# Performance work log

Measured on AMD Instinct MI355X. Metric: run time of the kernel, lower is better.

The kernel has to match this reference:

```python
import jax, jax.numpy as jnp
import numpy as np

D_MODEL = 512
NUM_HEADS = 8
HEAD_DIM = D_MODEL // NUM_HEADS  # 64
EMBEDDING_DIM = 512  # undefined global EmbeddingDim in source -> d_model
EVENT_DIM = 388      # undefined global EventDim in source -> MIDI event vocab
B, T = 2, 2048


def setup_inputs() -> dict:
    key = jax.random.key(0)
    ks = jax.random.split(key, 12)
    sc = 0.02
    v = jax.random.normal(ks[0], (B, T, D_MODEL), jnp.float32)
    k = jax.random.normal(ks[1], (B, T, D_MODEL), jnp.float32)
    q = jax.random.normal(ks[2], (B, T, D_MODEL), jnp.float32)
    mask = jnp.tril(jnp.ones((T, T), jnp.float32))  # causal mask, broadcasts to [H,B,T,T]
    Wq = jax.random.normal(ks[3], (D_MODEL, HEAD_DIM), jnp.float32) * sc
    bq = jnp.zeros((HEAD_DIM,), jnp.float32)
    Wk = jax.random.normal(ks[4], (D_MODEL, HEAD_DIM), jnp.float32) * sc
    bk = jnp.zeros((HEAD_DIM,), jnp.float32)
    Wv = jax.random.normal(ks[5], (D_MODEL, HEAD_DIM), jnp.float32) * sc
    bv = jnp.zeros((HEAD_DIM,), jnp.float32)
    E = jax.random.normal(ks[6], (NUM_HEADS, T, HEAD_DIM), jnp.float32) * sc
    Wo = jax.random.normal(ks[7], (D_MODEL, EMBEDDING_DIM), jnp.float32) * sc
    bo = jnp.zeros((EMBEDDING_DIM,), jnp.float32)
    Wl = jax.random.normal(ks[8], (EMBEDDING_DIM, EVENT_DIM), jnp.float32) * sc
    bl = jnp.zeros((EVENT_DIM,), jnp.float32)
    return {"v": v, "k": k, "q": q, "mask": mask, "Wq": Wq, "bq": bq,
            "Wk": Wk, "bk": bk, "Wv": Wv, "bv": bv, "E": E,
            "Wo": Wo, "bo": bo, "Wl": Wl, "bl": bl}


def _skew(S):
    # S: [H,B,T,T] -> Music-Transformer skew via left-pad, reshape, slice
    H, Bb, Tt, _ = S.shape
    S = jnp.pad(S, ((0, 0), (0, 0), (0, 0), (1, 0)))          # [H,B,T,T+1]
    S = S.reshape(H, Bb, Tt + 1, Tt)                           # [H,B,T+1,T]
    return S[:, :, 1:]                                         # [H,B,T,T]


def reference(v, k, q, mask, Wq, bq, Wk, bk, Wv, bv, E, Wo, bo, Wl, bl):
    # The source applies the SAME Dense per head, so all heads share q/k/v projections
    qh = q @ Wq + bq  # [B,T,hd]
    kh = k @ Wk + bk  # [B,T,hd]
    vh = v @ Wv + bv  # [B,T,hd]
    # relative-position scores per head: Q @ E^T then skew
    S = jnp.einsum('btd,hsd->hbts', qh, E)  # [H,B,T,T]
    S = _skew(S)
    qk = jnp.einsum('btd,bsd->bts', qh, kh)  # [B,T,T], identical across heads
    attn = (qk[None] + S) / np.sqrt(HEAD_DIM)  # [H,B,T,T]
    attn = attn * mask - jnp.asarray(1e10, attn.dtype) * (1.0 - mask)
    score = jax.nn.softmax(attn, axis=-1)
    ctx = jnp.einsum('hbts,bsd->hbtd', score, vh)  # [H,B,T,hd]
    ctx = jnp.transpose(ctx, (1, 2, 0, 3)).reshape(ctx.shape[1], ctx.shape[2], -1)  # [B,T,d_model]
    ctx = jax.nn.relu(ctx @ Wo + bo)  # [B,T,EmbeddingDim]
    logits = ctx @ Wl + bl            # [B,T,EventDim]
    return logits
```

## Files before the change

kernel.cpp:

```cpp
#include <hip/hip_runtime.h>
#include <hip/hip_bf16.h>


#define B_ 2
#define T_ 2048
#define DM_ 512
#define H_ 8
#define HD_ 64
#define ED_ 512
#define EV_ 388
#define BT_ (B_ * T_)

typedef __attribute__((ext_vector_type(8))) short short8;
typedef __attribute__((ext_vector_type(4))) float floatx4;

#define MFMA(a, b, c) __builtin_amdgcn_mfma_f32_16x16x32_bf16((a), (b), (c), 0, 0, 0)

__device__ __forceinline__ float bfs(unsigned short s) {
  union { unsigned int i; float f; } v; v.i = ((unsigned int)s) << 16; return v.f;
}
__device__ __forceinline__ unsigned short f2bf(float f) {
  __hip_bfloat16 h = __float2bfloat16(f);
  union { __hip_bfloat16 h; unsigned short u; } v; v.h = h; return v.u;
}
__device__ __forceinline__ float ldf(const void* p, int i, bool isbf) {
  return isbf ? bfs(((const unsigned short*)p)[i]) : ((const float*)p)[i];
}
__device__ __forceinline__ bool det_bf(const unsigned int* mask) {
  return mask[0] != 0x3F800000u;
}
__device__ __forceinline__ void gl_lds16(const unsigned short* g, void* l) {
  __builtin_amdgcn_global_load_lds(
      (const __attribute__((address_space(1))) void*)g,
      (__attribute__((address_space(3))) void*)l, 16, 0, 0);
}

__global__ __launch_bounds__(256) void prep_kernel(
    const void* __restrict__ E, const void* __restrict__ Wq,
    const void* __restrict__ Wk, const void* __restrict__ Wv,
    const void* __restrict__ Wo, const void* __restrict__ Wl,
    const unsigned int* __restrict__ mask,
    unsigned short* __restrict__ E_c, unsigned short* __restrict__ WqT,
    unsigned short* __restrict__ WkT, unsigned short* __restrict__ WvT,
    unsigned short* __restrict__ WoT, unsigned short* __restrict__ WlT) {
  const bool isbf = det_bf(mask);
  const int tid = threadIdx.x;
  int bi = blockIdx.x;
  if (bi < 1024) {
    const int i0 = (bi * 256 + tid) * 4;
    if (isbf) {
      *(uint2*)&E_c[i0] = *(const uint2*)((const unsigned short*)E + i0);
    } else {
      float4 f = *(const float4*)((const float*)E + i0);
      unsigned short p[4] = {f2bf(f.x), f2bf(f.y), f2bf(f.z), f2bf(f.w)};
      *(uint2*)&E_c[i0] = *(uint2*)p;
    }
    return;
  }
  bi -= 1024;
  const void* src; unsigned short* dst; int N, nb;
  if (bi < 16)       { src = Wq; dst = WqT; N = 64;  nb = bi; }
  else if (bi < 32)  { src = Wk; dst = WkT; N = 64;  nb = bi - 16; }
  else if (bi < 48)  { src = Wv; dst = WvT; N = 64;  nb = bi - 32; }
  else if (bi < 176) { src = Wo; dst = WoT; N = 512; nb = bi - 48; }
  else               { src = Wl; dst = WlT; N = 388; nb = bi - 176; }
  const int n = nb * 4 + (tid >> 6);
  const int k0 = (tid & 63) * 8;
  unsigned short vv[8];
#pragma unroll
  for (int j = 0; j < 8; ++j) {
    if (n >= N) vv[j] = 0;
    else if (isbf) vv[j] = ((const unsigned short*)src)[(size_t)(k0 + j) * N + n];
    else vv[j] = f2bf(((const float*)src)[(size_t)(k0 + j) * N + n]);
  }
  *(uint4*)&dst[(size_t)n * DM_ + k0] = *(uint4*)vv;
}

__global__ __launch_bounds__(256) void gemm_proj(
    const void* __restrict__ xq, const void* __restrict__ xk,
    const void* __restrict__ xv,
    const unsigned short* __restrict__ WqT, const unsigned short* __restrict__ WkT,
    const unsigned short* __restrict__ WvT,
    const void* __restrict__ bq, const void* __restrict__ bk,
    const void* __restrict__ bv, const unsigned int* __restrict__ mask,
    unsigned short* __restrict__ oq, unsigned short* __restrict__ ok,
    unsigned short* __restrict__ ovt) {
  __shared__ __align__(16) short sA[64][72];
  __shared__ __align__(16) short sW[64][72];
  const int sel = blockIdx.y;
  const void* x = (sel == 0) ? xq : (sel == 1) ? xk : xv;
  const unsigned short* WT = (sel == 0) ? WqT : (sel == 1) ? WkT : WvT;
  const void* bias = (sel == 0) ? bq : (sel == 1) ? bk : bv;
  const bool isbf = det_bf(mask);

  const int tid = threadIdx.x;
  const int w = tid >> 6, lane = tid & 63;
  const int q_ = lane >> 4, n_ = lane & 15;
  const int row0 = blockIdx.x * 64;

  floatx4 acc[4];
#pragma unroll
  for (int j = 0; j < 4; ++j) acc[j] = (floatx4){0.f, 0.f, 0.f, 0.f};

  for (int k0 = 0; k0 < DM_; k0 += 64) {
    if (isbf) {
#pragma unroll
      for (int it = 0; it < 2; ++it) {
        int idx = tid + it * 256;
        int rr = idx >> 3, cc = (idx & 7) * 8;
        *(uint4*)&sA[rr][cc] =
            *(const uint4*)((const unsigned short*)x + (size_t)(row0 + rr) * DM_ + k0 + cc);
      }
    } else {
#pragma unroll
      for (int it = 0; it < 4; ++it) {
        int idx = tid + it * 256;
        int rr = idx >> 4, cc = (idx & 15) * 4;
        float4 f = *(const float4*)((const float*)x + (size_t)(row0 + rr) * DM_ + k0 + cc);
        unsigned short p[4] = {f2bf(f.x), f2bf(f.y), f2bf(f.z), f2bf(f.w)};
        *(uint2*)&sA[rr][cc] = *(uint2*)p;
      }
    }
#pragma unroll
    for (int it = 0; it < 2; ++it) {
      int idx = tid + it * 256;
      int rr = idx >> 3, cc = (idx & 7) * 8;
      *(uint4*)&sW[rr][cc] = *(const uint4*)(WT + (size_t)rr * DM_ + k0 + cc);
    }
    __syncthreads();
    short8 a0 = *(const short8*)&sA[16 * w + n_][8 * q_];
    short8 a1 = *(const short8*)&sA[16 * w + n_][32 + 8 * q_];
#pragma unroll
    for (int nb = 0; nb < 4; ++nb) {
      short8 b0 = *(const short8*)&sW[16 * nb + n_][8 * q_];
      short8 b1 = *(const short8*)&sW[16 * nb + n_][32 + 8 * q_];
      acc[nb] = MFMA(a0, b0, acc[nb]);
      acc[nb] = MFMA(a1, b1, acc[nb]);
    }
    __syncthreads();
  }

#pragma unroll
  for (int nb = 0; nb < 4; ++nb) {
    const int col = 16 * nb + n_;
    const float bb = ldf(bias, col, isbf);
#pragma unroll
    for (int r = 0; r < 4; ++r) {
      int row = row0 + 16 * w + 4 * q_ + r;
      unsigned short val = f2bf(acc[nb][r] + bb);
      if (sel < 2) {
        unsigned short* o = (sel == 0) ? oq : ok;
        o[(size_t)row * HD_ + col] = val;
      } else {
        int b = row >> 11, s = row & 2047;
        ovt[(((size_t)(b * HD_ + col)) << 11) + s] = val;
      }
    }
  }
}

__device__ __forceinline__ int pbase_of(int ti) {
  return (ti < 16) ? (ti - 8) * 2 : (ti < 24) ? 16 + (ti - 16) * 3
                                              : 40 + (ti - 24) * 4;
}

__global__ __launch_bounds__(256, 2) void attn_kernel(
    const unsigned short* __restrict__ qh, const unsigned short* __restrict__ kh,
    const unsigned short* __restrict__ vt, const unsigned short* __restrict__ E,
    unsigned short* __restrict__ ctxo, float* __restrict__ pc,
    float* __restrict__ ml) {
  __shared__ __align__(16) short sK[2][64][64];
  __shared__ __align__(16) short sVT[2][64][64];
  __shared__ __align__(16) short sE[2][128][64];
  __shared__ __align__(16) short sP[64][64];

  const int id = blockIdx.x;
  const int hb = id & 15;
  const int rem = 79 - (id >> 4);
  int ti, c, nc;
  if (rem < 8)       { ti = rem;                 c = 0;            nc = 1; }
  else if (rem < 24) { ti = 8 + ((rem - 8) >> 1);  c = (rem - 8) & 1;  nc = 2; }
  else if (rem < 48) { ti = 16 + (rem - 24) / 3;   c = (rem - 24) % 3; nc = 3; }
  else               { ti = 24 + ((rem - 48) >> 2); c = (rem - 48) & 3; nc = 4; }
  const int nsteps = ti + 1;
  const int klo = (c * nsteps) / nc;
  const int khi = ((c + 1) * nsteps) / nc;

  const int h = hb >> 1, b = hb & 1;
  const int t0 = ti * 64;

  const int tid = threadIdx.x;
  const int w = tid >> 6, lane = tid & 63;
  const int q_ = lane >> 4, n_ = lane & 15;

  const int trow = t0 + 16 * w + n_;
  const unsigned short* qp = qh + (((size_t)((b << 11) + trow)) << 6) + (q_ << 3);
  const short8 qa0 = *(const short8*)qp;
  const short8 qa1 = *(const short8*)(qp + 32);

  short8 onesf;
#pragma unroll
  for (int j = 0; j < 8; ++j) onesf[j] = (short)0x3F80;

  floatx4 ctxa[4];
#pragma unroll
  for (int nb = 0; nb < 4; ++nb) ctxa[nb] = (floatx4){0.f, 0.f, 0.f, 0.f};
  floatx4 lacc = (floatx4){0.f, 0.f, 0.f, 0.f};

  const unsigned short* eb = E + ((size_t)h << 17);
  const unsigned short* kbase = kh + (((size_t)(b << 11)) << 6);
  const unsigned short* vbase = vt + (((size_t)(b << 6)) << 11);

  const int lrow8 = lane >> 3;
  const int lch = ((lane & 7) ^ lrow8) << 3;
  const int rK0 = 8 * w + lrow8;
  const int c0s = ((q_ ^ (n_ & 7)) << 3);
  const int c1s = (((q_ | 4) ^ (n_ & 7)) << 3);

#define STAGE(bufsel, s0v)                                                     \
  {                                                                            \
    const unsigned short* gK =                                                 \
        kbase + (((size_t)((s0v) + rK0)) << 6) + lch;                          \
    const unsigned short* gV =                                                 \
        vbase + (((size_t)rK0) << 11) + (s0v) + lch;                           \
    gl_lds16(gK, (void*)&sK[bufsel][8 * w][0]);                                \
    gl_lds16(gK + (32 << 6), (void*)(&sK[bufsel][8 * w][0] + 32 * 64));        \
    gl_lds16(gV, (void*)&sVT[bufsel][8 * w][0]);                               \
    gl_lds16(gV + (32 << 11), (void*)(&sVT[bufsel][8 * w][0] + 32 * 64));      \
    const int rbE = (T_ - 64) + (s0v)-t0;                                      \
    _Pragma("unroll") for (int off = 0; off < 4; ++off) {                      \
      int gr = rbE + 32 * w + 8 * off + lrow8;                                 \
      if (gr > T_ - 1) gr = T_ - 1;           \
      gl_lds16(eb + ((size_t)gr << 6) + lch,                                   \
               (void*)&sE[bufsel][32 * w + 8 * off][0]);                       \
    }                                                                          \
  }

  STAGE(0, klo * 64);

  for (int kt = klo; kt < khi; ++kt) {
    const int cur = (kt - klo) & 1;
    const int s0 = kt * 64;

    asm volatile("s_waitcnt vmcnt(0)" ::: "memory");
    __builtin_amdgcn_sched_barrier(0);
    __builtin_amdgcn_s_barrier();
    __builtin_amdgcn_sched_barrier(0);

    if (kt + 1 < khi) STAGE(cur ^ 1, s0 + 64);

    floatx4 qk[4];
    __builtin_amdgcn_s_setprio(1);
#pragma unroll
    for (int nb = 0; nb < 4; ++nb) {
      short8 kb0 = *(const short8*)&sK[cur][16 * nb + n_][c0s];
      short8 kb1 = *(const short8*)&sK[cur][16 * nb + n_][c1s];
      qk[nb] = (floatx4){0.f, 0.f, 0.f, 0.f};
      qk[nb] = MFMA(qa0, kb0, qk[nb]);
      qk[nb] = MFMA(qa1, kb1, qk[nb]);
    }
    floatx4 qe[5];
#pragma unroll
    for (int f = 0; f < 5; ++f) {
      const short* ep = &sE[cur][16 * (3 - w + f) + n_][0];
      short8 eb0 = *(const short8*)(ep + c0s);
      short8 eb1 = *(const short8*)(ep + c1s);
      qe[f] = (floatx4){0.f, 0.f, 0.f, 0.f};
      qe[f] = MFMA(qa0, eb0, qe[f]);
      qe[f] = MFMA(qa1, eb1, qe[f]);
    }
    __builtin_amdgcn_s_setprio(0);

    const bool diag = (kt == ti);
#pragma unroll
    for (int r = 0; r < 4; ++r) {
      const int t = 4 * q_ + r;
      const int ba = ((q_ << 4) | ((n_ - t + 15) & 15)) << 2;
      const int nd = (n_ + t + 1) & 15;
      const bool hi = nd > t;
      const int swr = (t & 7) << 3;
#pragma unroll
      for (int mb = 0; mb < 4; ++mb) {
        float merged = hi ? qe[mb + 1][r] : qe[mb][r];
        float g = __int_as_float(
            __builtin_amdgcn_ds_bpermute(ba, __float_as_int(merged)));
        float sv = qk[mb][r] + g;
        if (diag && (16 * mb + n_ > 16 * w + t)) sv = -1.0e30f;
        sP[16 * w + t][(16 * mb + n_) ^ swr] =
            (short)f2bf(exp2f(sv * 0.18033688011f));
      }
    }

    short8 pa0 = *(const short8*)&sP[16 * w + n_][c0s];
    short8 pa1 = *(const short8*)&sP[16 * w + n_][c1s];
    __builtin_amdgcn_s_setprio(1);
#pragma unroll
    for (int nb = 0; nb < 4; ++nb) {
      short8 v0 = *(const short8*)&sVT[cur][16 * nb + n_][c0s];
      short8 v1 = *(const short8*)&sVT[cur][16 * nb + n_][c1s];
      ctxa[nb] = MFMA(pa0, v0, ctxa[nb]);
      ctxa[nb] = MFMA(pa1, v1, ctxa[nb]);
    }
    lacc = MFMA(pa0, onesf, lacc);
    lacc = MFMA(pa1, onesf, lacc);
    __builtin_amdgcn_s_setprio(0);
  }
#undef STAGE

  if (nc == 1) {
#pragma unroll
    for (int r = 0; r < 4; ++r) {
      const float inv = 1.0f / lacc[r];
      const int row = t0 + 16 * w + 4 * q_ + r;
      const size_t base = (((size_t)((b << 11) + row)) << 9) + (h << 6) + n_;
#pragma unroll
      for (int nb = 0; nb < 4; ++nb)
        ctxo[base + 16 * nb] = f2bf(ctxa[nb][r] * inv);
    }
  } else {
    const int idx = hb * 72 + pbase_of(ti) + c;
    float* pcb = pc + ((size_t)idx << 12);
    float* mlb = ml + ((size_t)idx << 6);
#pragma unroll
    for (int r = 0; r < 4; ++r) {
      const int row = 16 * w + 4 * q_ + r;
#pragma unroll
      for (int nb = 0; nb < 4; ++nb)
        pcb[(row << 6) + 16 * nb + n_] = ctxa[nb][r];
      if (n_ == 0) mlb[row] = lacc[r];
    }
  }
}

__global__ __launch_bounds__(256) void combine_kernel(
    const float* __restrict__ pc, const float* __restrict__ ml,
    unsigned short* __restrict__ ctxo) {
  const int cb = blockIdx.x;
  const int hb = cb / 24;
  const int ti = 8 + cb % 24;
  const int nc = (ti >> 3) + 1;
  const int h = hb >> 1, b = hb & 1, t0 = ti * 64;
  const int tid = threadIdx.x;
  const int row = tid >> 2, seg = (tid & 3) * 16;
  const int idx0 = hb * 72 + pbase_of(ti);

  float lsum = 0.f;
  float4 a4[4];
#pragma unroll
  for (int j = 0; j < 4; ++j) a4[j] = (float4){0.f, 0.f, 0.f, 0.f};
  for (int c = 0; c < nc; ++c) {
    const int idx = idx0 + c;
    lsum += ml[((size_t)idx << 6) + row];
    const float* cp = pc + ((size_t)idx << 12) + (row << 6) + seg;
#pragma unroll
    for (int j = 0; j < 4; ++j) {
      float4 x = *(const float4*)(cp + 4 * j);
      a4[j].x += x.x; a4[j].y += x.y; a4[j].z += x.z; a4[j].w += x.w;
    }
  }
  const float inv = 1.0f / lsum;
  unsigned short o[16];
#pragma unroll
  for (int j = 0; j < 4; ++j) {
    o[4 * j + 0] = f2bf(a4[j].x * inv);
    o[4 * j + 1] = f2bf(a4[j].y * inv);
    o[4 * j + 2] = f2bf(a4[j].z * inv);
    o[4 * j + 3] = f2bf(a4[j].w * inv);
  }
  unsigned short* dst =
      ctxo + (((size_t)((b << 11) + t0 + row)) << 9) + (h << 6) + seg;
  *(uint4*)dst = *(uint4*)&o[0];
  *(uint4*)(dst + 8) = *(uint4*)&o[8];
}

template <int RELU>
__global__ __launch_bounds__(256) void mlp_mfma(
    const unsigned short* __restrict__ A, const unsigned short* __restrict__ WT,
    const void* __restrict__ bias, unsigned short* __restrict__ outBF,
    void* __restrict__ outD, const unsigned int* __restrict__ mask) {
  __shared__ __align__(16) short sA[64][72];
  __shared__ __align__(16) short sW[64][72];
  const int tid = threadIdx.x;
  const int w = tid >> 6, lane = tid & 63;
  const int q_ = lane >> 4, n_ = lane & 15;
  const int row0 = blockIdx.x * 64;
  const int n0 = blockIdx.y * 64;
  const bool isbf = det_bf(mask);

  floatx4 acc[4];
#pragma unroll
  for (int j = 0; j < 4; ++j) acc[j] = (floatx4){0.f, 0.f, 0.f, 0.f};

  for (int k0 = 0; k0 < DM_; k0 += 64) {
#pragma unroll
    for (int it = 0; it < 2; ++it) {
      int idx = tid + it * 256;
      int rr = idx >> 3, cc = (idx & 7) * 8;
      *(uint4*)&sA[rr][cc] = *(const uint4*)(A + (size_t)(row0 + rr) * DM_ + k0 + cc);
      *(uint4*)&sW[rr][cc] = *(const uint4*)(WT + (size_t)(n0 + rr) * DM_ + k0 + cc);
    }
    __syncthreads();
    short8 a0 = *(const short8*)&sA[16 * w + n_][8 * q_];
    short8 a1 = *(const short8*)&sA[16 * w + n_][32 + 8 * q_];
#pragma unroll
    for (int nb = 0; nb < 4; ++nb) {
      short8 b0 = *(const short8*)&sW[16 * nb + n_][8 * q_];
      short8 b1 = *(const short8*)&sW[16 * nb + n_][32 + 8 * q_];
      acc[nb] = MFMA(a0, b0, acc[nb]);
      acc[nb] = MFMA(a1, b1, acc[nb]);
    }
    __syncthreads();
  }

#pragma unroll
  for (int nb = 0; nb < 4; ++nb) {
    const int col = n0 + 16 * nb + n_;
    float bb = 0.f;
    if (RELU || col < EV_) bb = ldf(bias, col, isbf);
#pragma unroll
    for (int r = 0; r < 4; ++r) {
      const int row = row0 + 16 * w + 4 * q_ + r;
      float v = acc[nb][r] + bb;
      if (RELU) {
        outBF[(size_t)row * ED_ + col] = f2bf(fmaxf(v, 0.f));
      } else if (col < EV_) {
        if (isbf) ((unsigned short*)outD)[(size_t)row * EV_ + col] = f2bf(v);
        else      ((float*)outD)[(size_t)row * EV_ + col] = v;
      }
    }
  }
}

extern "C" void kernel_launch(void* const* d_in, const int* in_sizes, int n_in,
                              void* d_out, int out_size, void* d_ws, size_t ws_size,
                              hipStream_t stream) {
  const void* v  = d_in[0];
  const void* k  = d_in[1];
  const void* q  = d_in[2];
  const unsigned int* mask = (const unsigned int*)d_in[3];
  const void* Wq = d_in[4];
  const void* bq = d_in[5];
  const void* Wk = d_in[6];
  const void* bk = d_in[7];
  const void* Wv = d_in[8];
  const void* bv = d_in[9];
  const void* E  = d_in[10];
  const void* Wo = d_in[11];
  const void* bo = d_in[12];
  const void* Wl = d_in[13];
  const void* bl = d_in[14];

  char* p = (char*)d_ws;
  unsigned short* E_c  = (unsigned short*)p; p += (size_t)H_ * T_ * HD_ * 2;
  unsigned short* qhb  = (unsigned short*)p; p += (size_t)BT_ * HD_ * 2;
  unsigned short* khb  = (unsigned short*)p; p += (size_t)BT_ * HD_ * 2;
  unsigned short* vtb  = (unsigned short*)p; p += (size_t)BT_ * HD_ * 2;
  unsigned short* WqT  = (unsigned short*)p; p += (size_t)HD_ * DM_ * 2;
  unsigned short* WkT  = (unsigned short*)p; p += (size_t)HD_ * DM_ * 2;
  unsigned short* WvT  = (unsigned short*)p; p += (size_t)HD_ * DM_ * 2;
  unsigned short* WoT  = (unsigned short*)p; p += (size_t)ED_ * DM_ * 2;
  unsigned short* WlT  = (unsigned short*)p; p += (size_t)448 * DM_ * 2;
  unsigned short* ctxb = (unsigned short*)p; p += (size_t)BT_ * DM_ * 2;
  unsigned short* h1b  = (unsigned short*)p; p += (size_t)BT_ * ED_ * 2;
  float* pc = (float*)p; p += (size_t)16 * 72 * 4096 * 4;
  float* ml = (float*)p; p += (size_t)16 * 72 * 64 * 4;

  prep_kernel<<<dim3(1312), 256, 0, stream>>>(
      E, Wq, Wk, Wv, Wo, Wl, mask, E_c, WqT, WkT, WvT, WoT, WlT);
  gemm_proj<<<dim3(BT_ / 64, 3), 256, 0, stream>>>(
      q, k, v, WqT, WkT, WvT, bq, bk, bv, mask, qhb, khb, vtb);
  attn_kernel<<<dim3(1280), 256, 0, stream>>>(qhb, khb, vtb, E_c, ctxb, pc, ml);
  combine_kernel<<<dim3(384), 256, 0, stream>>>(pc, ml, ctxb);
  mlp_mfma<1><<<dim3(BT_ / 64, ED_ / 64), 256, 0, stream>>>(
      ctxb, WoT, bo, h1b, nullptr, mask);
  mlp_mfma<0><<<dim3(BT_ / 64, 448 / 64), 256, 0, stream>>>(
      h1b, WlT, bl, nullptr, d_out, mask);
}
```

Measured before the change: 202.5 us.

## Load K/V fragments directly from global and rebalance attention split-K partitioning

K and V^T fragments are now read straight from global memory into registers instead of being staged through double-buffered LDS, which shrinks LDS use and lets the launch bound rise to 4 blocks per SM. The split-K partitioning of query tiles is reworked to at most 3 chunks, and block order is no longer reversed to launch the longest tiles first, so fewer blocks and a smaller partial buffer feed the combine kernel. The risk is higher global and L2 traffic and latency exposed on every MFMA operand load, since nothing prefetches these loads now, and worse tail balance.

After: 235.9 us. 1.17x slower.

```diff
diff --git a/kernel.cpp b/kernel.cpp
--- a/kernel.cpp
+++ b/kernel.cpp
@@ -160,28 +160,24 @@
 }
 
 __device__ __forceinline__ int pbase_of(int ti) {
-  return (ti < 16) ? (ti - 8) * 2 : (ti < 24) ? 16 + (ti - 16) * 3
-                                              : 40 + (ti - 24) * 4;
-}
-
-__global__ __launch_bounds__(256, 2) void attn_kernel(
+  return (ti < 22) ? (ti - 11) * 2 : 22 + (ti - 22) * 3;
+}
+
+__global__ __launch_bounds__(256, 4) void attn_kernel(
     const unsigned short* __restrict__ qh, const unsigned short* __restrict__ kh,
     const unsigned short* __restrict__ vt, const unsigned short* __restrict__ E,
     unsigned short* __restrict__ ctxo, float* __restrict__ pc,
     float* __restrict__ ml) {
-  __shared__ __align__(16) short sK[2][64][64];
-  __shared__ __align__(16) short sVT[2][64][64];
   __shared__ __align__(16) short sE[2][128][64];
   __shared__ __align__(16) short sP[64][64];
 
   const int id = blockIdx.x;
   const int hb = id & 15;
-  const int rem = 79 - (id >> 4);
+  const int rem = id >> 4;
   int ti, c, nc;
-  if (rem < 8)       { ti = rem;                 c = 0;            nc = 1; }
-  else if (rem < 24) { ti = 8 + ((rem - 8) >> 1);  c = (rem - 8) & 1;  nc = 2; }
-  else if (rem < 48) { ti = 16 + (rem - 24) / 3;   c = (rem - 24) % 3; nc = 3; }
-  else               { ti = 24 + ((rem - 48) >> 2); c = (rem - 48) & 3; nc = 4; }
+  if (rem < 11)      { ti = rem;                  c = 0;              nc = 1; }
+  else if (rem < 33) { ti = 11 + ((rem - 11) >> 1); c = (rem - 11) & 1; nc = 2; }
+  else               { ti = 22 + (rem - 33) / 3;    c = (rem - 33) % 3; nc = 3; }
   const int nsteps = ti + 1;
   const int klo = (c * nsteps) / nc;
   const int khi = ((c + 1) * nsteps) / nc;
@@ -208,25 +204,16 @@
   floatx4 lacc = (floatx4){0.f, 0.f, 0.f, 0.f};
 
   const unsigned short* eb = E + ((size_t)h << 17);
-  const unsigned short* kbase = kh + (((size_t)(b << 11)) << 6);
-  const unsigned short* vbase = vt + (((size_t)(b << 6)) << 11);
+  const unsigned short* kfr = kh + (((size_t)(b << 11) + n_) << 6) + (q_ << 3);
+  const unsigned short* vfr = vt + (((size_t)((b << 6) + n_)) << 11) + (q_ << 3);
 
   const int lrow8 = lane >> 3;
   const int lch = ((lane & 7) ^ lrow8) << 3;
-  const int rK0 = 8 * w + lrow8;
   const int c0s = ((q_ ^ (n_ & 7)) << 3);
   const int c1s = (((q_ | 4) ^ (n_ & 7)) << 3);
 
 #define STAGE(bufsel, s0v)                                                     \
   {                                                                            \
-    const unsigned short* gK =                                                 \
-        kbase + (((size_t)((s0v) + rK0)) << 6) + lch;                          \
-    const unsigned short* gV =                                                 \
-        vbase + (((size_t)rK0) << 11) + (s0v) + lch;                           \
-    gl_lds16(gK, (void*)&sK[bufsel][8 * w][0]);                                \
-    gl_lds16(gK + (32 << 6), (void*)(&sK[bufsel][8 * w][0] + 32 * 64));        \
-    gl_lds16(gV, (void*)&sVT[bufsel][8 * w][0]);                               \
-    gl_lds16(gV + (32 << 11), (void*)(&sVT[bufsel][8 * w][0] + 32 * 64));      \
     const int rbE = (T_ - 64) + (s0v)-t0;                                      \
     _Pragma("unroll") for (int off = 0; off < 4; ++off) {                      \
       int gr = rbE + 32 * w + 8 * off + lrow8;                                 \
@@ -253,8 +240,9 @@
     __builtin_amdgcn_s_setprio(1);
 #pragma unroll
     for (int nb = 0; nb < 4; ++nb) {
-      short8 kb0 = *(const short8*)&sK[cur][16 * nb + n_][c0s];
-      short8 kb1 = *(const short8*)&sK[cur][16 * nb + n_][c1s];
+      const unsigned short* kp = kfr + (((size_t)(s0 + 16 * nb)) << 6);
+      short8 kb0 = *(const short8*)kp;
+      short8 kb1 = *(const short8*)(kp + 32);
       qk[nb] = (floatx4){0.f, 0.f, 0.f, 0.f};
       qk[nb] = MFMA(qa0, kb0, qk[nb]);
       qk[nb] = MFMA(qa1, kb1, qk[nb]);
@@ -296,8 +284,9 @@
     __builtin_amdgcn_s_setprio(1);
 #pragma unroll
     for (int nb = 0; nb < 4; ++nb) {
-      short8 v0 = *(const short8*)&sVT[cur][16 * nb + n_][c0s];
-      short8 v1 = *(const short8*)&sVT[cur][16 * nb + n_][c1s];
+      const unsigned short* vp = vfr + (((size_t)(16 * nb)) << 11) + s0;
+      short8 v0 = *(const short8*)vp;
+      short8 v1 = *(const short8*)(vp + 32);
       ctxa[nb] = MFMA(pa0, v0, ctxa[nb]);
       ctxa[nb] = MFMA(pa1, v1, ctxa[nb]);
     }
@@ -318,7 +307,7 @@
         ctxo[base + 16 * nb] = f2bf(ctxa[nb][r] * inv);
     }
   } else {
-    const int idx = hb * 72 + pbase_of(ti) + c;
+    const int idx = hb * 52 + pbase_of(ti) + c;
     float* pcb = pc + ((size_t)idx << 12);
     float* mlb = ml + ((size_t)idx << 6);
 #pragma unroll
@@ -336,13 +325,13 @@
     const float* __restrict__ pc, const float* __restrict__ ml,
     unsigned short* __restrict__ ctxo) {
   const int cb = blockIdx.x;
-  const int hb = cb / 24;
-  const int ti = 8 + cb % 24;
-  const int nc = (ti >> 3) + 1;
+  const int hb = cb / 21;
+  const int ti = 11 + cb % 21;
+  const int nc = (ti < 22) ? 2 : 3;
   const int h = hb >> 1, b = hb & 1, t0 = ti * 64;
   const int tid = threadIdx.x;
   const int row = tid >> 2, seg = (tid & 3) * 16;
-  const int idx0 = hb * 72 + pbase_of(ti);
+  const int idx0 = hb * 52 + pbase_of(ti);
 
   float lsum = 0.f;
   float4 a4[4];
@@ -462,15 +451,15 @@
   unsigned short* WlT  = (unsigned short*)p; p += (size_t)448 * DM_ * 2;
   unsigned short* ctxb = (unsigned short*)p; p += (size_t)BT_ * DM_ * 2;
   unsigned short* h1b  = (unsigned short*)p; p += (size_t)BT_ * ED_ * 2;
-  float* pc = (float*)p; p += (size_t)16 * 72 * 4096 * 4;
-  float* ml = (float*)p; p += (size_t)16 * 72 * 64 * 4;
+  float* pc = (float*)p; p += (size_t)16 * 52 * 4096 * 4;
+  float* ml = (float*)p; p += (size_t)16 * 52 * 64 * 4;
 
   prep_kernel<<<dim3(1312), 256, 0, stream>>>(
       E, Wq, Wk, Wv, Wo, Wl, mask, E_c, WqT, WkT, WvT, WoT, WlT);
   gemm_proj<<<dim3(BT_ / 64, 3), 256, 0, stream>>>(
       q, k, v, WqT, WkT, WvT, bq, bk, bv, mask, qhb, khb, vtb);
-  attn_kernel<<<dim3(1280), 256, 0, stream>>>(qhb, khb, vtb, E_c, ctxb, pc, ml);
-  combine_kernel<<<dim3(384), 256, 0, stream>>>(pc, ml, ctxb);
+  attn_kernel<<<dim3(1008), 256, 0, stream>>>(qhb, khb, vtb, E_c, ctxb, pc, ml);
+  combine_kernel<<<dim3(336), 256, 0, stream>>>(pc, ml, ctxb);
   mlp_mfma<1><<<dim3(BT_ / 64, ED_ / 64), 256, 0, stream>>>(
       ctxb, WoT, bo, h1b, nullptr, mask);
   mlp_mfma<0><<<dim3(BT_ / 64, 448 / 64), 256, 0, stream>>>(
```

## Software-pipeline PV MFMA one tile behind QK/QE with triple-buffered V

Applied to the files above, without the earlier changes.

Defers the P·V and row-sum MFMAs of each key tile into the next iteration, issuing them alongside that iteration's QK and QE MFMAs, with a drain step after the loop. V^T gets a third LDS buffer so the previous tile's V stays resident while the next one is prefetched. The aim is to overlap the exp/softmax VALU work with matrix-core work and hide the LDS read latency of the P tile. It costs extra LDS, which may reduce occupancy, adds modulo-3 indexing, and keeps the P fragments live in registers across iterations.

New measurement: 206.7 us. 1.02x slower.

```diff
diff --git a/kernel.cpp b/kernel.cpp
--- a/kernel.cpp
+++ b/kernel.cpp
@@ -170,7 +170,7 @@
     unsigned short* __restrict__ ctxo, float* __restrict__ pc,
     float* __restrict__ ml) {
   __shared__ __align__(16) short sK[2][64][64];
-  __shared__ __align__(16) short sVT[2][64][64];
+  __shared__ __align__(16) short sVT[3][64][64];
   __shared__ __align__(16) short sE[2][128][64];
   __shared__ __align__(16) short sP[64][64];
 
@@ -217,29 +217,33 @@
   const int c0s = ((q_ ^ (n_ & 7)) << 3);
   const int c1s = (((q_ | 4) ^ (n_ & 7)) << 3);
 
-#define STAGE(bufsel, s0v)                                                     \
+#define STAGE(kbuf, vbuf, s0v)                                                 \
   {                                                                            \
     const unsigned short* gK =                                                 \
         kbase + (((size_t)((s0v) + rK0)) << 6) + lch;                          \
     const unsigned short* gV =                                                 \
         vbase + (((size_t)rK0) << 11) + (s0v) + lch;                           \
-    gl_lds16(gK, (void*)&sK[bufsel][8 * w][0]);                                \
-    gl_lds16(gK + (32 << 6), (void*)(&sK[bufsel][8 * w][0] + 32 * 64));        \
-    gl_lds16(gV, (void*)&sVT[bufsel][8 * w][0]);                               \
-    gl_lds16(gV + (32 << 11), (void*)(&sVT[bufsel][8 * w][0] + 32 * 64));      \
+    gl_lds16(gK, (void*)&sK[kbuf][8 * w][0]);                                  \
+    gl_lds16(gK + (32 << 6), (void*)(&sK[kbuf][8 * w][0] + 32 * 64));          \
+    gl_lds16(gV, (void*)&sVT[vbuf][8 * w][0]);                                 \
+    gl_lds16(gV + (32 << 11), (void*)(&sVT[vbuf][8 * w][0] + 32 * 64));        \
     const int rbE = (T_ - 64) + (s0v)-t0;                                      \
     _Pragma("unroll") for (int off = 0; off < 4; ++off) {                      \
       int gr = rbE + 32 * w + 8 * off + lrow8;                                 \
       if (gr > T_ - 1) gr = T_ - 1;           \
       gl_lds16(eb + ((size_t)gr << 6) + lch,                                   \
-               (void*)&sE[bufsel][32 * w + 8 * off][0]);                       \
+               (void*)&sE[kbuf][32 * w + 8 * off][0]);                         \
     }                                                                          \
   }
 
-  STAGE(0, klo * 64);
+  STAGE(0, 0, klo * 64);
+
+  short8 pa0p = {0, 0, 0, 0, 0, 0, 0, 0};
+  short8 pa1p = {0, 0, 0, 0, 0, 0, 0, 0};
 
   for (int kt = klo; kt < khi; ++kt) {
-    const int cur = (kt - klo) & 1;
+    const int ph = (kt - klo) & 1;
+    const int vcur = (kt - klo) % 3;
     const int s0 = kt * 64;
 
     asm volatile("s_waitcnt vmcnt(0)" ::: "memory");
@@ -247,14 +251,14 @@
     __builtin_amdgcn_s_barrier();
     __builtin_amdgcn_sched_barrier(0);
 
-    if (kt + 1 < khi) STAGE(cur ^ 1, s0 + 64);
+    if (kt + 1 < khi) STAGE(ph ^ 1, (kt + 1 - klo) % 3, s0 + 64);
 
     floatx4 qk[4];
     __builtin_amdgcn_s_setprio(1);
 #pragma unroll
     for (int nb = 0; nb < 4; ++nb) {
-      short8 kb0 = *(const short8*)&sK[cur][16 * nb + n_][c0s];
-      short8 kb1 = *(const short8*)&sK[cur][16 * nb + n_][c1s];
+      short8 kb0 = *(const short8*)&sK[ph][16 * nb + n_][c0s];
+      short8 kb1 = *(const short8*)&sK[ph][16 * nb + n_][c1s];
       qk[nb] = (floatx4){0.f, 0.f, 0.f, 0.f};
       qk[nb] = MFMA(qa0, kb0, qk[nb]);
       qk[nb] = MFMA(qa1, kb1, qk[nb]);
@@ -262,12 +266,24 @@
     floatx4 qe[5];
 #pragma unroll
     for (int f = 0; f < 5; ++f) {
-      const short* ep = &sE[cur][16 * (3 - w + f) + n_][0];
+      const short* ep = &sE[ph][16 * (3 - w + f) + n_][0];
       short8 eb0 = *(const short8*)(ep + c0s);
       short8 eb1 = *(const short8*)(ep + c1s);
       qe[f] = (floatx4){0.f, 0.f, 0.f, 0.f};
       qe[f] = MFMA(qa0, eb0, qe[f]);
       qe[f] = MFMA(qa1, eb1, qe[f]);
+    }
+    if (kt > klo) {
+      const int vprev = (vcur + 2) % 3;
+#pragma unroll
+      for (int nb = 0; nb < 4; ++nb) {
+        short8 v0 = *(const short8*)&sVT[vprev][16 * nb + n_][c0s];
+        short8 v1 = *(const short8*)&sVT[vprev][16 * nb + n_][c1s];
+        ctxa[nb] = MFMA(pa0p, v0, ctxa[nb]);
+        ctxa[nb] = MFMA(pa1p, v1, ctxa[nb]);
+      }
+      lacc = MFMA(pa0p, onesf, lacc);
+      lacc = MFMA(pa1p, onesf, lacc);
     }
     __builtin_amdgcn_s_setprio(0);
 
@@ -291,21 +307,25 @@
       }
     }
 
-    short8 pa0 = *(const short8*)&sP[16 * w + n_][c0s];
-    short8 pa1 = *(const short8*)&sP[16 * w + n_][c1s];
+    pa0p = *(const short8*)&sP[16 * w + n_][c0s];
+    pa1p = *(const short8*)&sP[16 * w + n_][c1s];
+  }
+#undef STAGE
+
+  {
+    const int vlast = (khi - 1 - klo) % 3;
     __builtin_amdgcn_s_setprio(1);
 #pragma unroll
     for (int nb = 0; nb < 4; ++nb) {
-      short8 v0 = *(const short8*)&sVT[cur][16 * nb + n_][c0s];
-      short8 v1 = *(const short8*)&sVT[cur][16 * nb + n_][c1s];
-      ctxa[nb] = MFMA(pa0, v0, ctxa[nb]);
-      ctxa[nb] = MFMA(pa1, v1, ctxa[nb]);
-    }
-    lacc = MFMA(pa0, onesf, lacc);
-    lacc = MFMA(pa1, onesf, lacc);
+      short8 v0 = *(const short8*)&sVT[vlast][16 * nb + n_][c0s];
+      short8 v1 = *(const short8*)&sVT[vlast][16 * nb + n_][c1s];
+      ctxa[nb] = MFMA(pa0p, v0, ctxa[nb]);
+      ctxa[nb] = MFMA(pa1p, v1, ctxa[nb]);
+    }
+    lacc = MFMA(pa0p, onesf, lacc);
+    lacc = MFMA(pa1p, onesf, lacc);
     __builtin_amdgcn_s_setprio(0);
   }
-#undef STAGE
 
   if (nc == 1) {
 #pragma unroll
```
